# Kernel optimization log

Measured on AMD Instinct MI355X. Metric: run time of the kernel, lower is better.

The kernel has to match this reference:

```python
import jax, jax.numpy as jnp
import numpy as np

E, D, H, K = 8, 2048, 1024, 2  # num_experts, input_size, hidden_size, top_k
B, L = 2, 1024


def setup_inputs() -> dict:
    key = jax.random.key(0)
    k1, k2, k3, k4 = jax.random.split(key, 4)
    x = jax.random.normal(k1, (B, L, D), dtype=jnp.float32)
    w_gate = jax.random.normal(k2, (E, D), dtype=jnp.float32) * 0.02   # router Linear weight [E, D]
    w_in = jax.random.normal(k3, (E, 2 * H, D), dtype=jnp.float32) * 0.02  # ParallelExperts [E, out=2H, in=D]
    w_out = jax.random.normal(k4, (E, D, H), dtype=jnp.float32) * 0.02     # ParallelExperts [E, out=D, in=H]
    bias = jnp.zeros((D,), dtype=jnp.float32)
    return {"x": x, "w_gate": w_gate, "w_in": w_in, "w_out": w_out, "bias": bias}


def _moe_forward(x, w_gate, w_in, w_out, bias):
    bsz, length, d = x.shape
    xt = x.reshape(-1, d)  # [T, D]
    # top-k router: logits -> top-k -> softmax over selected logits
    logits = xt @ w_gate.T  # [T, E]
    topk_vals, topk_idx = jax.lax.top_k(logits, K)  # [T, K]
    topk_gates = jax.nn.softmax(topk_vals, axis=-1)  # [T, K]
    T = xt.shape[0]
    # dense [T, E] gate matrix; zero for non-selected experts, so the dense
    # per-expert compute below is mathematically identical to gathered dispatch
    gates = jnp.zeros((T, E), dtype=xt.dtype).at[jnp.arange(T)[:, None], topk_idx].add(topk_gates)
    # expert GLU FFN, vectorized over experts
    h = jnp.einsum('td,efd->tef', xt, w_in)  # [T, E, 2H]
    h1, h2 = jnp.split(h, 2, axis=-1)
    a = jax.nn.silu(h1) * h2                 # [T, E, H]
    eo = jnp.einsum('teh,edh->ted', a, w_out)  # [T, E, D]
    y = jnp.einsum('ted,te->td', eo, gates) + bias
    return y.reshape(bsz, length, d)


def reference(x, w_gate, w_in, w_out, bias):
    y = _moe_forward(x, w_gate, w_in, w_out, bias)
    loss = jnp.float32(0.0)  # router aux loss is 0 in eval mode (JetMoE top_k_gating)
    return (y, loss)
```

## Files before the change

### kernel.cpp

```cpp
#include <hip/hip_runtime.h>
#include <hip/hip_bf16.h>

#define E_    8
#define D_    2048
#define H_    1024
#define T_    2048
#define BK    64

using u16   = unsigned short;
using s16x8 = __attribute__((ext_vector_type(8))) short;
using f32x4 = __attribute__((ext_vector_type(4))) float;

__device__ __forceinline__ short f2bf(float f) {
  __hip_bfloat16 h = __float2bfloat16(f);
  return __builtin_bit_cast(short, h);
}
__device__ __forceinline__ s16x8 cvt8(f32x4 a, f32x4 b) {
  s16x8 o;
  o[0]=f2bf(a.x); o[1]=f2bf(a.y); o[2]=f2bf(a.z); o[3]=f2bf(a.w);
  o[4]=f2bf(b.x); o[5]=f2bf(b.y); o[6]=f2bf(b.z); o[7]=f2bf(b.w);
  return o;
}
__device__ __forceinline__ int slot(int r, int c) { return r * 64 + ((c ^ (r & 7)) << 3); }

__device__ __forceinline__ void gload16(const void* g, void* l) {
  __builtin_amdgcn_global_load_lds((const __attribute__((address_space(1))) void*)g,
                                   (__attribute__((address_space(3))) void*)l, 16, 0, 0);
}

#define FIND_EXPERT(ml, cnt, e, mt, Ne)                        \
  { int b_ = 0;                                                \
    _Pragma("unroll")                                          \
    for (int i_ = 0; i_ < E_; ++i_) {                          \
      int ti_ = (cnt[i_] + 255) >> 8;                          \
      if ((ml) >= b_ && (ml) < b_ + ti_) {                     \
        e = i_; mt = (ml) - b_; Ne = cnt[i_]; }                \
      b_ += ti_; } }


__global__ __launch_bounds__(256) void init_kernel(
    const float* __restrict__ bias, float* __restrict__ out, int* __restrict__ counts)
{
  int idx = blockIdx.x * 256 + threadIdx.x;
  if (blockIdx.x == 0 && threadIdx.x < E_) counts[threadIdx.x] = 0;
  if (idx == 0) out[(size_t)T_ * D_] = 0.0f;
  int dq = idx & (D_ / 4 - 1);
  f32x4 b = *(const f32x4*)(bias + dq * 4);
  *(f32x4*)(out + (size_t)idx * 4) = b;
}

__global__ __launch_bounds__(256) void router_kernel(
    const float* __restrict__ x, const float* __restrict__ wg,
    u16* __restrict__ xb, int* __restrict__ lists, float* __restrict__ gates,
    int* __restrict__ counts)
{
  int t = blockIdx.x;
  int tid = threadIdx.x;
  const float* xr = x + (size_t)t * D_;
  float acc[E_];
#pragma unroll
  for (int e = 0; e < E_; ++e) acc[e] = 0.f;
#pragma unroll
  for (int i = 0; i < D_ / 256; ++i) {
    int d = tid + 256 * i;
    float xv = xr[d];
    xb[(size_t)t * D_ + d] = (u16)f2bf(xv);
#pragma unroll
    for (int e = 0; e < E_; ++e) acc[e] += xv * wg[e * D_ + d];
  }
#pragma unroll
  for (int off = 32; off >= 1; off >>= 1)
#pragma unroll
    for (int e = 0; e < E_; ++e) acc[e] += __shfl_down(acc[e], off);

  __shared__ float red[4][E_];
  int w = tid >> 6, lane = tid & 63;
  if (lane == 0)
#pragma unroll
    for (int e = 0; e < E_; ++e) red[w][e] = acc[e];
  __syncthreads();
  if (tid == 0) {
    float v0 = -1e30f, v1 = -1e30f; int e0 = 0, e1 = 0;
#pragma unroll
    for (int e = 0; e < E_; ++e) {
      float v = red[0][e] + red[1][e] + red[2][e] + red[3][e];
      if (v > v0)      { v1 = v0; e1 = e0; v0 = v; e0 = e; }
      else if (v > v1) { v1 = v;  e1 = e; }
    }
    float g1 = expf(v1 - v0);
    float inv = 1.f / (1.f + g1);
    float g0 = inv; g1 *= inv;
    int s0 = atomicAdd(&counts[e0], 1);
    lists[e0 * T_ + s0] = t * 2 + 0;
    gates[t * 2 + 0] = g0;
    int s1 = atomicAdd(&counts[e1], 1);
    lists[e1 * T_ + s1] = t * 2 + 1;
    gates[t * 2 + 1] = g1;
  }
}

__global__ __launch_bounds__(512, 2) void gemm1_kernel(
    const u16* __restrict__ xb, const float* __restrict__ w_in,
    const int* __restrict__ lists, const int* __restrict__ counts,
    u16* __restrict__ a_buf)
{
  __shared__ __align__(16) u16 As[2][256 * 64];
  __shared__ __align__(16) u16 Bs[2][128 * 64];

  int cnt[E_];
#pragma unroll
  for (int i = 0; i < E_; ++i) cnt[i] = counts[i];
  int mt_total = 0;
#pragma unroll
  for (int i = 0; i < E_; ++i) mt_total += (cnt[i] + 255) >> 8;
  const int NN1 = 2 * H_ / 128;
  int total = mt_total * NN1;
  int chunk = (total + 7) >> 3;

  int tid = threadIdx.x, w = tid >> 6, lane = tid & 63;
  int swzc = ((lane & 7) ^ (lane >> 3)) * 8;
  int sr = tid >> 3;
  int brow = tid >> 2, bc = (tid & 3) * 2;
  int wr = (w >> 1) * 64, wcB = (w & 1) * 64, lrow = lane & 15, g = lane >> 4;
  int lcol = lane & 15, lr4 = (lane >> 4) * 4;

  int xcd = blockIdx.x & 7, bslot = blockIdx.x >> 3;

  for (int sl = bslot; sl < chunk; sl += 32) {
    int t = xcd * chunk + sl;
    if (t >= total) break;
    int ml = t / NN1, n = t % NN1;
    int e = 0, mt = 0, Ne = 0;
    FIND_EXPERT(ml, cnt, e, mt, Ne);

    const u16* ap[4];
#pragma unroll
    for (int i = 0; i < 4; ++i) {
      int gr = mt * 256 + 32 * w + 8 * i + (lane >> 3);
      if (gr >= Ne) gr = Ne - 1;
      ap[i] = xb + (size_t)(lists[e * T_ + gr] >> 1) * D_ + swzc;
    }
    int o = n * 64 + ((brow >> 4) & 1) * H_ + (brow >> 5) * 16 + (brow & 15);
    const float* bp = w_in + (size_t)e * (2 * H_) * D_ + (size_t)o * D_ + bc * 8;

    f32x4 acc[4][4];
#pragma unroll
    for (int m = 0; m < 4; ++m)
#pragma unroll
      for (int nn = 0; nn < 4; ++nn) acc[m][nn] = (f32x4){0.f, 0.f, 0.f, 0.f};

    f32x4 bl[4];
#define LOADS1(K) { _Pragma("unroll") for (int j = 0; j < 4; ++j) \
                      bl[j] = *(const f32x4*)(bp + (K) + j * 4); \
                    _Pragma("unroll") for (int i = 0; i < 4; ++i) \
                      gload16(ap[i] + (K), &As[(K) ? !((K/BK) & 1) : 0][(32 * w + 8 * i) * 64]); }
    { _Pragma("unroll") for (int j = 0; j < 4; ++j) bl[j] = *(const f32x4*)(bp + j * 4);
      _Pragma("unroll") for (int i = 0; i < 4; ++i) gload16(ap[i], &As[0][(32 * w + 8 * i) * 64]); }
    *(s16x8*)(&Bs[0][slot(brow, bc)])     = cvt8(bl[0], bl[1]);
    *(s16x8*)(&Bs[0][slot(brow, bc + 1)]) = cvt8(bl[2], bl[3]);
    __syncthreads();

    const int NT = D_ / BK;
    for (int kt = 0; kt < NT; ++kt) {
      int cur = kt & 1;
      if (kt + 1 < NT) {
        int k = (kt + 1) * BK;
#pragma unroll
        for (int j = 0; j < 4; ++j) bl[j] = *(const f32x4*)(bp + k + j * 4);
#pragma unroll
        for (int i = 0; i < 4; ++i) gload16(ap[i] + k, &As[cur ^ 1][(32 * w + 8 * i) * 64]);
      }
#pragma unroll
      for (int ks = 0; ks < 2; ++ks) {
        int ch = ks * 4 + g;
        s16x8 af[4], bf[4];
#pragma unroll
        for (int m = 0; m < 4; ++m) af[m] = *(const s16x8*)(&As[cur][slot(wr + m * 16 + lrow, ch)]);
#pragma unroll
        for (int nn = 0; nn < 4; ++nn) bf[nn] = *(const s16x8*)(&Bs[cur][slot(wcB + nn * 16 + lrow, ch)]);
#pragma unroll
        for (int m = 0; m < 4; ++m)
#pragma unroll
          for (int nn = 0; nn < 4; ++nn)
            acc[m][nn] = __builtin_amdgcn_mfma_f32_16x16x32_bf16(af[m], bf[nn], acc[m][nn], 0, 0, 0);
      }
      if (kt + 1 < NT) {
        *(s16x8*)(&Bs[cur ^ 1][slot(brow, bc)])     = cvt8(bl[0], bl[1]);
        *(s16x8*)(&Bs[cur ^ 1][slot(brow, bc + 1)]) = cvt8(bl[2], bl[3]);
      }
      __syncthreads();
    }
#pragma unroll
    for (int m = 0; m < 4; ++m)
#pragma unroll
      for (int q = 0; q < 4; ++q) {
        int row = mt * 256 + wr + m * 16 + lr4 + q;
        if (row < Ne) {
#pragma unroll
          for (int n2 = 0; n2 < 2; ++n2) {
            float h1 = acc[m][n2 * 2][q], h2 = acc[m][n2 * 2 + 1][q];
            float a = (h1 / (1.f + __expf(-h1))) * h2;
            int col = n * 64 + ((w & 1) * 2 + n2) * 16 + lcol;
            a_buf[((size_t)e * T_ + row) * H_ + col] = (u16)f2bf(a);
          }
        }
      }
  }
}

__global__ __launch_bounds__(512, 2) void gemm2_kernel(
    const u16* __restrict__ a_buf, const float* __restrict__ w_out,
    const int* __restrict__ lists, const int* __restrict__ counts,
    const float* __restrict__ gates, float* __restrict__ out)
{
  __shared__ __align__(16) u16 As[2][256 * 64];
  __shared__ __align__(16) u16 Bs[2][128 * 64];

  int cnt[E_];
#pragma unroll
  for (int i = 0; i < E_; ++i) cnt[i] = counts[i];
  int mt_total = 0;
#pragma unroll
  for (int i = 0; i < E_; ++i) mt_total += (cnt[i] + 255) >> 8;
  const int NN2 = D_ / 128;
  int total = mt_total * NN2;
  int chunk = (total + 7) >> 3;

  int tid = threadIdx.x, w = tid >> 6, lane = tid & 63;
  int swzc = ((lane & 7) ^ (lane >> 3)) * 8;
  int brow = tid >> 2, bc = (tid & 3) * 2;
  int wr = (w >> 1) * 64, wcB = (w & 1) * 64, lrow = lane & 15, g = lane >> 4;
  int lcol = lane & 15, lr4 = (lane >> 4) * 4;

  int xcd = blockIdx.x & 7, bslot = blockIdx.x >> 3;

  for (int sl = bslot; sl < chunk; sl += 32) {
    int t = xcd * chunk + sl;
    if (t >= total) break;
    int ml = t / NN2, n = t % NN2;
    int e = 0, mt = 0, Ne = 0;
    FIND_EXPERT(ml, cnt, e, mt, Ne);

    const u16* ap[4];
#pragma unroll
    for (int i = 0; i < 4; ++i) {
      int gr = mt * 256 + 32 * w + 8 * i + (lane >> 3);
      if (gr >= Ne) gr = Ne - 1;
      ap[i] = a_buf + ((size_t)e * T_ + gr) * H_ + swzc;
    }
    const float* bp = w_out + (size_t)e * D_ * H_ + (size_t)(n * 128 + brow) * H_ + bc * 8;

    f32x4 acc[4][4];
#pragma unroll
    for (int m = 0; m < 4; ++m)
#pragma unroll
      for (int nn = 0; nn < 4; ++nn) acc[m][nn] = (f32x4){0.f, 0.f, 0.f, 0.f};

    f32x4 bl[4];
    { _Pragma("unroll") for (int j = 0; j < 4; ++j) bl[j] = *(const f32x4*)(bp + j * 4);
      _Pragma("unroll") for (int i = 0; i < 4; ++i) gload16(ap[i], &As[0][(32 * w + 8 * i) * 64]); }
    *(s16x8*)(&Bs[0][slot(brow, bc)])     = cvt8(bl[0], bl[1]);
    *(s16x8*)(&Bs[0][slot(brow, bc + 1)]) = cvt8(bl[2], bl[3]);
    __syncthreads();

    const int NT = H_ / BK;
    for (int kt = 0; kt < NT; ++kt) {
      int cur = kt & 1;
      if (kt + 1 < NT) {
        int k = (kt + 1) * BK;
#pragma unroll
        for (int j = 0; j < 4; ++j) bl[j] = *(const f32x4*)(bp + k + j * 4);
#pragma unroll
        for (int i = 0; i < 4; ++i) gload16(ap[i] + k, &As[cur ^ 1][(32 * w + 8 * i) * 64]);
      }
#pragma unroll
      for (int ks = 0; ks < 2; ++ks) {
        int ch = ks * 4 + g;
        s16x8 af[4], bf[4];
#pragma unroll
        for (int m = 0; m < 4; ++m) af[m] = *(const s16x8*)(&As[cur][slot(wr + m * 16 + lrow, ch)]);
#pragma unroll
        for (int nn = 0; nn < 4; ++nn) bf[nn] = *(const s16x8*)(&Bs[cur][slot(wcB + nn * 16 + lrow, ch)]);
#pragma unroll
        for (int m = 0; m < 4; ++m)
#pragma unroll
          for (int nn = 0; nn < 4; ++nn)
            acc[m][nn] = __builtin_amdgcn_mfma_f32_16x16x32_bf16(af[m], bf[nn], acc[m][nn], 0, 0, 0);
      }
      if (kt + 1 < NT) {
        *(s16x8*)(&Bs[cur ^ 1][slot(brow, bc)])     = cvt8(bl[0], bl[1]);
        *(s16x8*)(&Bs[cur ^ 1][slot(brow, bc + 1)]) = cvt8(bl[2], bl[3]);
      }
      __syncthreads();
    }
#pragma unroll
    for (int m = 0; m < 4; ++m)
#pragma unroll
      for (int q = 0; q < 4; ++q) {
        int row = mt * 256 + wr + m * 16 + lr4 + q;
        if (row < Ne) {
          int p = lists[e * T_ + row];
          float gt = gates[p];
          int tok = p >> 1;
#pragma unroll
          for (int nn = 0; nn < 4; ++nn)
            atomicAdd(&out[(size_t)tok * D_ + n * 128 + wcB + nn * 16 + lcol], gt * acc[m][nn][q]);
        }
      }
  }
}

extern "C" void kernel_launch(void* const* d_in, const int* in_sizes, int n_in,
                              void* d_out, int out_size, void* d_ws, size_t ws_size,
                              hipStream_t stream)
{
  const float* x      = (const float*)d_in[0];
  const float* w_gate = (const float*)d_in[1];
  const float* w_in   = (const float*)d_in[2];
  const float* w_out  = (const float*)d_in[3];
  const float* bias   = (const float*)d_in[4];
  float* out = (float*)d_out;

  char* ws = (char*)d_ws;
  u16*   xb     = (u16*)(ws);
  u16*   a_buf  = (u16*)(ws + 8388608);
  int*   lists  = (int*)(ws + 41943040);
  float* gates  = (float*)(ws + 42008576);
  int*   counts = (int*)(ws + 42024960);

  init_kernel<<<T_ * D_ / 4 / 256, 256, 0, stream>>>(bias, out, counts);
  router_kernel<<<T_, 256, 0, stream>>>(x, w_gate, xb, lists, gates, counts);
  gemm1_kernel<<<256, 512, 0, stream>>>(xb, w_in, lists, counts, a_buf);
  gemm2_kernel<<<256, 512, 0, stream>>>(a_buf, w_out, lists, counts, gates, out);
}
```

Before: 265.8 us.

## Triple-buffer A tiles with explicit waitcnt scheduling and retile both MoE GEMMs

Both expert GEMMs now use a three-stage LDS ring for the activation tiles, prefetching two K-steps ahead. Plain __syncthreads is replaced with manual vmcnt/lgkmcnt waits, sched barriers, s_barrier and setprio around the MFMA bursts, so loads overlap compute. The wave tiling changes so each wave covers more rows and fewer columns, gemm2 drops to 128-row M tiles, and its grid doubles to 512 blocks. gemm1 launch bounds fall to one block per CU because of the larger LDS, which lowers occupancy and relies on the hand-tuned wait counts being correct.

```diff
diff --git a/kernel.cpp b/kernel.cpp
--- a/kernel.cpp
+++ b/kernel.cpp
@@ -11,6 +11,10 @@
 using s16x8 = __attribute__((ext_vector_type(8))) short;
 using f32x4 = __attribute__((ext_vector_type(4))) float;
 
+#define WAITVM(N) asm volatile("s_waitcnt vmcnt(" #N ")" ::: "memory")
+#define LGKM0     asm volatile("s_waitcnt lgkmcnt(0)" ::: "memory")
+#define SB0       __builtin_amdgcn_sched_barrier(0)
+
 __device__ __forceinline__ short f2bf(float f) {
   __hip_bfloat16 h = __float2bfloat16(f);
   return __builtin_bit_cast(short, h);
@@ -28,11 +32,11 @@
                                    (__attribute__((address_space(3))) void*)l, 16, 0, 0);
 }
 
-#define FIND_EXPERT(ml, cnt, e, mt, Ne)                        \
+#define FIND_EXPERT(ml, cnt, e, mt, Ne, RND, SH)               \
   { int b_ = 0;                                                \
     _Pragma("unroll")                                          \
     for (int i_ = 0; i_ < E_; ++i_) {                          \
-      int ti_ = (cnt[i_] + 255) >> 8;                          \
+      int ti_ = (cnt[i_] + RND) >> SH;                         \
       if ((ml) >= b_ && (ml) < b_ + ti_) {                     \
         e = i_; mt = (ml) - b_; Ne = cnt[i_]; }                \
       b_ += ti_; } }
@@ -99,12 +103,12 @@
   }
 }
 
-__global__ __launch_bounds__(512, 2) void gemm1_kernel(
+__global__ __launch_bounds__(512, 1) void gemm1_kernel(
     const u16* __restrict__ xb, const float* __restrict__ w_in,
     const int* __restrict__ lists, const int* __restrict__ counts,
     u16* __restrict__ a_buf)
 {
-  __shared__ __align__(16) u16 As[2][256 * 64];
+  __shared__ __align__(16) u16 As[3][256 * 64];
   __shared__ __align__(16) u16 Bs[2][128 * 64];
 
   int cnt[E_];
@@ -113,25 +117,22 @@
   int mt_total = 0;
 #pragma unroll
   for (int i = 0; i < E_; ++i) mt_total += (cnt[i] + 255) >> 8;
-  const int NN1 = 2 * H_ / 128;
-  int total = mt_total * NN1;
+  int total = mt_total * 16;
   int chunk = (total + 7) >> 3;
 
   int tid = threadIdx.x, w = tid >> 6, lane = tid & 63;
   int swzc = ((lane & 7) ^ (lane >> 3)) * 8;
-  int sr = tid >> 3;
   int brow = tid >> 2, bc = (tid & 3) * 2;
-  int wr = (w >> 1) * 64, wcB = (w & 1) * 64, lrow = lane & 15, g = lane >> 4;
+  int wr = (w >> 2) * 128, wc = (w & 3) * 32, lrow = lane & 15, g = lane >> 4;
   int lcol = lane & 15, lr4 = (lane >> 4) * 4;
-
   int xcd = blockIdx.x & 7, bslot = blockIdx.x >> 3;
 
   for (int sl = bslot; sl < chunk; sl += 32) {
     int t = xcd * chunk + sl;
     if (t >= total) break;
-    int ml = t / NN1, n = t % NN1;
+    int ml = t >> 4, n = t & 15;
     int e = 0, mt = 0, Ne = 0;
-    FIND_EXPERT(ml, cnt, e, mt, Ne);
+    FIND_EXPERT(ml, cnt, e, mt, Ne, 255, 8);
 
     const u16* ap[4];
 #pragma unroll
@@ -143,66 +144,85 @@
     int o = n * 64 + ((brow >> 4) & 1) * H_ + (brow >> 5) * 16 + (brow & 15);
     const float* bp = w_in + (size_t)e * (2 * H_) * D_ + (size_t)o * D_ + bc * 8;
 
-    f32x4 acc[4][4];
-#pragma unroll
-    for (int m = 0; m < 4; ++m)
-#pragma unroll
-      for (int nn = 0; nn < 4; ++nn) acc[m][nn] = (f32x4){0.f, 0.f, 0.f, 0.f};
-
+    f32x4 acc[8][2];
+#pragma unroll
+    for (int m = 0; m < 8; ++m) { acc[m][0] = (f32x4){0,0,0,0}; acc[m][1] = (f32x4){0,0,0,0}; }
     f32x4 bl[4];
-#define LOADS1(K) { _Pragma("unroll") for (int j = 0; j < 4; ++j) \
-                      bl[j] = *(const f32x4*)(bp + (K) + j * 4); \
-                    _Pragma("unroll") for (int i = 0; i < 4; ++i) \
-                      gload16(ap[i] + (K), &As[(K) ? !((K/BK) & 1) : 0][(32 * w + 8 * i) * 64]); }
-    { _Pragma("unroll") for (int j = 0; j < 4; ++j) bl[j] = *(const f32x4*)(bp + j * 4);
-      _Pragma("unroll") for (int i = 0; i < 4; ++i) gload16(ap[i], &As[0][(32 * w + 8 * i) * 64]); }
+
+#pragma unroll
+    for (int j = 0; j < 4; ++j) bl[j] = *(const f32x4*)(bp + j * 4);
+    SB0;
+#pragma unroll
+    for (int i = 0; i < 4; ++i) gload16(ap[i], &As[0][(32 * w + 8 * i) * 64]);
+    SB0;
+#pragma unroll
+    for (int i = 0; i < 4; ++i) gload16(ap[i] + BK, &As[1][(32 * w + 8 * i) * 64]);
+    SB0;
+    WAITVM(8);  SB0;
     *(s16x8*)(&Bs[0][slot(brow, bc)])     = cvt8(bl[0], bl[1]);
     *(s16x8*)(&Bs[0][slot(brow, bc + 1)]) = cvt8(bl[2], bl[3]);
-    __syncthreads();
+    SB0;
+#pragma unroll
+    for (int j = 0; j < 4; ++j) bl[j] = *(const f32x4*)(bp + BK + j * 4);
+    SB0;
+    WAITVM(8);  SB0;
+    LGKM0;
+    __builtin_amdgcn_s_barrier();
 
     const int NT = D_ / BK;
     for (int kt = 0; kt < NT; ++kt) {
-      int cur = kt & 1;
-      if (kt + 1 < NT) {
-        int k = (kt + 1) * BK;
-#pragma unroll
-        for (int j = 0; j < 4; ++j) bl[j] = *(const f32x4*)(bp + k + j * 4);
-#pragma unroll
-        for (int i = 0; i < 4; ++i) gload16(ap[i] + k, &As[cur ^ 1][(32 * w + 8 * i) * 64]);
+      int cur = kt % 3;
+      if (kt + 2 < NT) {
+        int wrt = cur + 2; if (wrt >= 3) wrt -= 3;
+        int k2 = (kt + 2) * BK;
+        SB0;
+#pragma unroll
+        for (int i = 0; i < 4; ++i) gload16(ap[i] + k2, &As[wrt][(32 * w + 8 * i) * 64]);
+        SB0;
       }
 #pragma unroll
       for (int ks = 0; ks < 2; ++ks) {
         int ch = ks * 4 + g;
-        s16x8 af[4], bf[4];
-#pragma unroll
-        for (int m = 0; m < 4; ++m) af[m] = *(const s16x8*)(&As[cur][slot(wr + m * 16 + lrow, ch)]);
-#pragma unroll
-        for (int nn = 0; nn < 4; ++nn) bf[nn] = *(const s16x8*)(&Bs[cur][slot(wcB + nn * 16 + lrow, ch)]);
-#pragma unroll
-        for (int m = 0; m < 4; ++m)
-#pragma unroll
-          for (int nn = 0; nn < 4; ++nn)
+        s16x8 af[8], bf[2];
+#pragma unroll
+        for (int m = 0; m < 8; ++m) af[m] = *(const s16x8*)(&As[cur][slot(wr + m * 16 + lrow, ch)]);
+        bf[0] = *(const s16x8*)(&Bs[kt & 1][slot(wc + lrow, ch)]);
+        bf[1] = *(const s16x8*)(&Bs[kt & 1][slot(wc + 16 + lrow, ch)]);
+        __builtin_amdgcn_s_setprio(1);
+#pragma unroll
+        for (int m = 0; m < 8; ++m)
+#pragma unroll
+          for (int nn = 0; nn < 2; ++nn)
             acc[m][nn] = __builtin_amdgcn_mfma_f32_16x16x32_bf16(af[m], bf[nn], acc[m][nn], 0, 0, 0);
+        __builtin_amdgcn_s_setprio(0);
       }
       if (kt + 1 < NT) {
-        *(s16x8*)(&Bs[cur ^ 1][slot(brow, bc)])     = cvt8(bl[0], bl[1]);
-        *(s16x8*)(&Bs[cur ^ 1][slot(brow, bc + 1)]) = cvt8(bl[2], bl[3]);
-      }
-      __syncthreads();
-    }
-#pragma unroll
-    for (int m = 0; m < 4; ++m)
+        if (kt + 2 < NT) { WAITVM(4); } else { WAITVM(0); }
+        SB0;
+        *(s16x8*)(&Bs[(kt + 1) & 1][slot(brow, bc)])     = cvt8(bl[0], bl[1]);
+        *(s16x8*)(&Bs[(kt + 1) & 1][slot(brow, bc + 1)]) = cvt8(bl[2], bl[3]);
+        SB0;
+        if (kt + 2 < NT) {
+          int k2 = (kt + 2) * BK;
+#pragma unroll
+          for (int j = 0; j < 4; ++j) bl[j] = *(const f32x4*)(bp + k2 + j * 4);
+          SB0;
+        }
+        LGKM0;
+        __builtin_amdgcn_s_barrier();
+      }
+    }
+    LGKM0;
+    __builtin_amdgcn_s_barrier();
+#pragma unroll
+    for (int m = 0; m < 8; ++m)
 #pragma unroll
       for (int q = 0; q < 4; ++q) {
         int row = mt * 256 + wr + m * 16 + lr4 + q;
         if (row < Ne) {
-#pragma unroll
-          for (int n2 = 0; n2 < 2; ++n2) {
-            float h1 = acc[m][n2 * 2][q], h2 = acc[m][n2 * 2 + 1][q];
-            float a = (h1 / (1.f + __expf(-h1))) * h2;
-            int col = n * 64 + ((w & 1) * 2 + n2) * 16 + lcol;
-            a_buf[((size_t)e * T_ + row) * H_ + col] = (u16)f2bf(a);
-          }
+          float h1 = acc[m][0][q], h2 = acc[m][1][q];
+          float a = (h1 / (1.f + __expf(-h1))) * h2;
+          a_buf[((size_t)e * T_ + row) * H_ + n * 64 + (w & 3) * 16 + lcol] = (u16)f2bf(a);
         }
       }
   }
@@ -213,7 +233,7 @@
     const int* __restrict__ lists, const int* __restrict__ counts,
     const float* __restrict__ gates, float* __restrict__ out)
 {
-  __shared__ __align__(16) u16 As[2][256 * 64];
+  __shared__ __align__(16) u16 As[3][128 * 64];
   __shared__ __align__(16) u16 Bs[2][128 * 64];
 
   int cnt[E_];
@@ -221,90 +241,115 @@
   for (int i = 0; i < E_; ++i) cnt[i] = counts[i];
   int mt_total = 0;
 #pragma unroll
-  for (int i = 0; i < E_; ++i) mt_total += (cnt[i] + 255) >> 8;
-  const int NN2 = D_ / 128;
-  int total = mt_total * NN2;
+  for (int i = 0; i < E_; ++i) mt_total += (cnt[i] + 127) >> 7;
+  int total = mt_total * 16;
   int chunk = (total + 7) >> 3;
 
   int tid = threadIdx.x, w = tid >> 6, lane = tid & 63;
   int swzc = ((lane & 7) ^ (lane >> 3)) * 8;
   int brow = tid >> 2, bc = (tid & 3) * 2;
-  int wr = (w >> 1) * 64, wcB = (w & 1) * 64, lrow = lane & 15, g = lane >> 4;
+  int wr = (w >> 2) * 64, wc = (w & 3) * 32, lrow = lane & 15, g = lane >> 4;
   int lcol = lane & 15, lr4 = (lane >> 4) * 4;
-
   int xcd = blockIdx.x & 7, bslot = blockIdx.x >> 3;
 
-  for (int sl = bslot; sl < chunk; sl += 32) {
+  for (int sl = bslot; sl < chunk; sl += 64) {
     int t = xcd * chunk + sl;
     if (t >= total) break;
-    int ml = t / NN2, n = t % NN2;
+    int ml = t >> 4, n = t & 15;
     int e = 0, mt = 0, Ne = 0;
-    FIND_EXPERT(ml, cnt, e, mt, Ne);
-
-    const u16* ap[4];
-#pragma unroll
-    for (int i = 0; i < 4; ++i) {
-      int gr = mt * 256 + 32 * w + 8 * i + (lane >> 3);
+    FIND_EXPERT(ml, cnt, e, mt, Ne, 127, 7);
+
+    const u16* ap[2];
+#pragma unroll
+    for (int i = 0; i < 2; ++i) {
+      int gr = mt * 128 + 16 * w + 8 * i + (lane >> 3);
       if (gr >= Ne) gr = Ne - 1;
       ap[i] = a_buf + ((size_t)e * T_ + gr) * H_ + swzc;
     }
     const float* bp = w_out + (size_t)e * D_ * H_ + (size_t)(n * 128 + brow) * H_ + bc * 8;
 
-    f32x4 acc[4][4];
-#pragma unroll
-    for (int m = 0; m < 4; ++m)
-#pragma unroll
-      for (int nn = 0; nn < 4; ++nn) acc[m][nn] = (f32x4){0.f, 0.f, 0.f, 0.f};
-
+    f32x4 acc[4][2];
+#pragma unroll
+    for (int m = 0; m < 4; ++m) { acc[m][0] = (f32x4){0,0,0,0}; acc[m][1] = (f32x4){0,0,0,0}; }
     f32x4 bl[4];
-    { _Pragma("unroll") for (int j = 0; j < 4; ++j) bl[j] = *(const f32x4*)(bp + j * 4);
-      _Pragma("unroll") for (int i = 0; i < 4; ++i) gload16(ap[i], &As[0][(32 * w + 8 * i) * 64]); }
+
+#pragma unroll
+    for (int j = 0; j < 4; ++j) bl[j] = *(const f32x4*)(bp + j * 4);
+    SB0;
+#pragma unroll
+    for (int i = 0; i < 2; ++i) gload16(ap[i], &As[0][(16 * w + 8 * i) * 64]);
+    SB0;
+#pragma unroll
+    for (int i = 0; i < 2; ++i) gload16(ap[i] + BK, &As[1][(16 * w + 8 * i) * 64]);
+    SB0;
+    WAITVM(4);  SB0;
     *(s16x8*)(&Bs[0][slot(brow, bc)])     = cvt8(bl[0], bl[1]);
     *(s16x8*)(&Bs[0][slot(brow, bc + 1)]) = cvt8(bl[2], bl[3]);
-    __syncthreads();
+    SB0;
+#pragma unroll
+    for (int j = 0; j < 4; ++j) bl[j] = *(const f32x4*)(bp + BK + j * 4);
+    SB0;
+    WAITVM(6);  SB0;
+    LGKM0;
+    __builtin_amdgcn_s_barrier();
 
     const int NT = H_ / BK;
     for (int kt = 0; kt < NT; ++kt) {
-      int cur = kt & 1;
-      if (kt + 1 < NT) {
-        int k = (kt + 1) * BK;
-#pragma unroll
-        for (int j = 0; j < 4; ++j) bl[j] = *(const f32x4*)(bp + k + j * 4);
-#pragma unroll
-        for (int i = 0; i < 4; ++i) gload16(ap[i] + k, &As[cur ^ 1][(32 * w + 8 * i) * 64]);
+      int cur = kt % 3;
+      if (kt + 2 < NT) {
+        int wrt = cur + 2; if (wrt >= 3) wrt -= 3;
+        int k2 = (kt + 2) * BK;
+        SB0;
+#pragma unroll
+        for (int i = 0; i < 2; ++i) gload16(ap[i] + k2, &As[wrt][(16 * w + 8 * i) * 64]);
+        SB0;
       }
 #pragma unroll
       for (int ks = 0; ks < 2; ++ks) {
         int ch = ks * 4 + g;
-        s16x8 af[4], bf[4];
+        s16x8 af[4], bf[2];
 #pragma unroll
         for (int m = 0; m < 4; ++m) af[m] = *(const s16x8*)(&As[cur][slot(wr + m * 16 + lrow, ch)]);
-#pragma unroll
-        for (int nn = 0; nn < 4; ++nn) bf[nn] = *(const s16x8*)(&Bs[cur][slot(wcB + nn * 16 + lrow, ch)]);
+        bf[0] = *(const s16x8*)(&Bs[kt & 1][slot(wc + lrow, ch)]);
+        bf[1] = *(const s16x8*)(&Bs[kt & 1][slot(wc + 16 + lrow, ch)]);
+        __builtin_amdgcn_s_setprio(1);
 #pragma unroll
         for (int m = 0; m < 4; ++m)
 #pragma unroll
-          for (int nn = 0; nn < 4; ++nn)
+          for (int nn = 0; nn < 2; ++nn)
             acc[m][nn] = __builtin_amdgcn_mfma_f32_16x16x32_bf16(af[m], bf[nn], acc[m][nn], 0, 0, 0);
+        __builtin_amdgcn_s_setprio(0);
       }
       if (kt + 1 < NT) {
-        *(s16x8*)(&Bs[cur ^ 1][slot(brow, bc)])     = cvt8(bl[0], bl[1]);
-        *(s16x8*)(&Bs[cur ^ 1][slot(brow, bc + 1)]) = cvt8(bl[2], bl[3]);
-      }
-      __syncthreads();
-    }
+        if (kt + 2 < NT) { WAITVM(2); } else { WAITVM(0); }
+        SB0;
+        *(s16x8*)(&Bs[(kt + 1) & 1][slot(brow, bc)])     = cvt8(bl[0], bl[1]);
+        *(s16x8*)(&Bs[(kt + 1) & 1][slot(brow, bc + 1)]) = cvt8(bl[2], bl[3]);
+        SB0;
+        if (kt + 2 < NT) {
+          int k2 = (kt + 2) * BK;
+#pragma unroll
+          for (int j = 0; j < 4; ++j) bl[j] = *(const f32x4*)(bp + k2 + j * 4);
+          SB0;
+        }
+        LGKM0;
+        __builtin_amdgcn_s_barrier();
+      }
+    }
+    LGKM0;
+    __builtin_amdgcn_s_barrier();
 #pragma unroll
     for (int m = 0; m < 4; ++m)
 #pragma unroll
       for (int q = 0; q < 4; ++q) {
-        int row = mt * 256 + wr + m * 16 + lr4 + q;
+        int row = mt * 128 + wr + m * 16 + lr4 + q;
         if (row < Ne) {
           int p = lists[e * T_ + row];
           float gt = gates[p];
           int tok = p >> 1;
 #pragma unroll
-          for (int nn = 0; nn < 4; ++nn)
-            atomicAdd(&out[(size_t)tok * D_ + n * 128 + wcB + nn * 16 + lcol], gt * acc[m][nn][q]);
+          for (int nn = 0; nn < 2; ++nn)
+            atomicAdd(&out[(size_t)tok * D_ + n * 128 + wc + nn * 16 + lcol], gt * acc[m][nn][q]);
         }
       }
   }
@@ -331,5 +376,5 @@
   init_kernel<<<T_ * D_ / 4 / 256, 256, 0, stream>>>(bias, out, counts);
   router_kernel<<<T_, 256, 0, stream>>>(x, w_gate, xb, lists, gates, counts);
   gemm1_kernel<<<256, 512, 0, stream>>>(xb, w_in, lists, counts, a_buf);
-  gemm2_kernel<<<256, 512, 0, stream>>>(a_buf, w_out, lists, counts, gates, out);
-}
+  gemm2_kernel<<<512, 512, 0, stream>>>(a_buf, w_out, lists, counts, gates, out);
+}
```

New measurement: 231.7 us. -12.8%, faster.

## Shrink GEMM M-tiles to 128, add dynamic work queue, fold init into router

Applied to the files above, without the earlier changes.

Both expert GEMMs now use 128-row M tiles with 256-thread blocks (double the grid) and pull tiles from a per-XCD atomic work queue instead of a static stride. Adjacent M-tiles are interleaved so they share the same weight N-tile. The bias/output init kernel is removed: the router writes the bias rows and a memset clears the counters and queues. The aim is less padding waste per expert and better load balance across uneven expert counts, at the cost of less A/B reuse per tile and extra atomic and barrier traffic.

```diff
diff --git a/kernel.cpp b/kernel.cpp
--- a/kernel.cpp
+++ b/kernel.cpp
@@ -11,6 +11,8 @@
 using s16x8 = __attribute__((ext_vector_type(8))) short;
 using f32x4 = __attribute__((ext_vector_type(4))) float;
 
+#define WAITVM0 asm volatile("s_waitcnt vmcnt(0)" ::: "memory")
+
 __device__ __forceinline__ short f2bf(float f) {
   __hip_bfloat16 h = __float2bfloat16(f);
   return __builtin_bit_cast(short, h);
@@ -32,30 +34,29 @@
   { int b_ = 0;                                                \
     _Pragma("unroll")                                          \
     for (int i_ = 0; i_ < E_; ++i_) {                          \
-      int ti_ = (cnt[i_] + 255) >> 8;                          \
+      int ti_ = (cnt[i_] + 127) >> 7;                          \
       if ((ml) >= b_ && (ml) < b_ + ti_) {                     \
         e = i_; mt = (ml) - b_; Ne = cnt[i_]; }                \
       b_ += ti_; } }
 
 
-__global__ __launch_bounds__(256) void init_kernel(
-    const float* __restrict__ bias, float* __restrict__ out, int* __restrict__ counts)
-{
-  int idx = blockIdx.x * 256 + threadIdx.x;
-  if (blockIdx.x == 0 && threadIdx.x < E_) counts[threadIdx.x] = 0;
-  if (idx == 0) out[(size_t)T_ * D_] = 0.0f;
-  int dq = idx & (D_ / 4 - 1);
-  f32x4 b = *(const f32x4*)(bias + dq * 4);
-  *(f32x4*)(out + (size_t)idx * 4) = b;
-}
-
 __global__ __launch_bounds__(256) void router_kernel(
     const float* __restrict__ x, const float* __restrict__ wg,
+    const float* __restrict__ bias,
     u16* __restrict__ xb, int* __restrict__ lists, float* __restrict__ gates,
-    int* __restrict__ counts)
+    int* __restrict__ counts, float* __restrict__ out)
 {
   int t = blockIdx.x;
   int tid = threadIdx.x;
+
+  {
+    const float* bp = bias + tid * 8;
+    f32x4 b0 = *(const f32x4*)(bp), b1 = *(const f32x4*)(bp + 4);
+    *(f32x4*)(out + (size_t)t * D_ + tid * 8)     = b0;
+    *(f32x4*)(out + (size_t)t * D_ + tid * 8 + 4) = b1;
+    if (t == 0 && tid == 0) out[(size_t)T_ * D_] = 0.0f;
+  }
+
   const float* xr = x + (size_t)t * D_;
   float acc[E_];
 #pragma unroll
@@ -99,65 +100,70 @@
   }
 }
 
-__global__ __launch_bounds__(512, 2) void gemm1_kernel(
+__global__ __launch_bounds__(256, 2) void gemm1_kernel(
     const u16* __restrict__ xb, const float* __restrict__ w_in,
     const int* __restrict__ lists, const int* __restrict__ counts,
-    u16* __restrict__ a_buf)
+    u16* __restrict__ a_buf, int* __restrict__ q)
 {
-  __shared__ __align__(16) u16 As[2][256 * 64];
+  __shared__ __align__(16) u16 As[2][128 * 64];
   __shared__ __align__(16) u16 Bs[2][128 * 64];
+  __shared__ int s_sl;
 
   int cnt[E_];
 #pragma unroll
   for (int i = 0; i < E_; ++i) cnt[i] = counts[i];
   int mt_total = 0;
 #pragma unroll
-  for (int i = 0; i < E_; ++i) mt_total += (cnt[i] + 255) >> 8;
-  const int NN1 = 2 * H_ / 128;
-  int total = mt_total * NN1;
+  for (int i = 0; i < E_; ++i) mt_total += (cnt[i] + 127) >> 7;
+  int total = ((mt_total + 1) >> 1) * 32;
   int chunk = (total + 7) >> 3;
 
   int tid = threadIdx.x, w = tid >> 6, lane = tid & 63;
   int swzc = ((lane & 7) ^ (lane >> 3)) * 8;
-  int sr = tid >> 3;
-  int brow = tid >> 2, bc = (tid & 3) * 2;
-  int wr = (w >> 1) * 64, wcB = (w & 1) * 64, lrow = lane & 15, g = lane >> 4;
+  int wr = (w >> 1) * 64, wc = (w & 1) * 64, lrow = lane & 15, g = lane >> 4;
   int lcol = lane & 15, lr4 = (lane >> 4) * 4;
-
-  int xcd = blockIdx.x & 7, bslot = blockIdx.x >> 3;
-
-  for (int sl = bslot; sl < chunk; sl += 32) {
+  int br = tid >> 1, bhalf = (tid & 1) * 32, bj0 = (tid & 1) * 4;
+  int xcd = blockIdx.x & 7;
+
+  for (;;) {
+    __syncthreads();
+    if (tid == 0) s_sl = atomicAdd(&q[xcd], 1);
+    __syncthreads();
+    int sl = s_sl;
+    if (sl >= chunk) break;
     int t = xcd * chunk + sl;
     if (t >= total) break;
-    int ml = t / NN1, n = t % NN1;
+    int p = t >> 5, qq = t & 31;
+    int ml = p * 2 + (qq & 1), n = qq >> 1;
+    if (ml >= mt_total) continue;
     int e = 0, mt = 0, Ne = 0;
     FIND_EXPERT(ml, cnt, e, mt, Ne);
 
     const u16* ap[4];
 #pragma unroll
     for (int i = 0; i < 4; ++i) {
-      int gr = mt * 256 + 32 * w + 8 * i + (lane >> 3);
+      int gr = mt * 128 + w * 32 + i * 8 + (lane >> 3);
       if (gr >= Ne) gr = Ne - 1;
       ap[i] = xb + (size_t)(lists[e * T_ + gr] >> 1) * D_ + swzc;
     }
-    int o = n * 64 + ((brow >> 4) & 1) * H_ + (brow >> 5) * 16 + (brow & 15);
-    const float* bp = w_in + (size_t)e * (2 * H_) * D_ + (size_t)o * D_ + bc * 8;
+    int o = n * 64 + ((br >> 4) & 1) * H_ + (br >> 5) * 16 + (br & 15);
+    const float* bp = w_in + (size_t)e * (2 * H_) * D_ + (size_t)o * D_ + bhalf;
 
     f32x4 acc[4][4];
 #pragma unroll
     for (int m = 0; m < 4; ++m)
 #pragma unroll
       for (int nn = 0; nn < 4; ++nn) acc[m][nn] = (f32x4){0.f, 0.f, 0.f, 0.f};
-
-    f32x4 bl[4];
-#define LOADS1(K) { _Pragma("unroll") for (int j = 0; j < 4; ++j) \
-                      bl[j] = *(const f32x4*)(bp + (K) + j * 4); \
-                    _Pragma("unroll") for (int i = 0; i < 4; ++i) \
-                      gload16(ap[i] + (K), &As[(K) ? !((K/BK) & 1) : 0][(32 * w + 8 * i) * 64]); }
-    { _Pragma("unroll") for (int j = 0; j < 4; ++j) bl[j] = *(const f32x4*)(bp + j * 4);
-      _Pragma("unroll") for (int i = 0; i < 4; ++i) gload16(ap[i], &As[0][(32 * w + 8 * i) * 64]); }
-    *(s16x8*)(&Bs[0][slot(brow, bc)])     = cvt8(bl[0], bl[1]);
-    *(s16x8*)(&Bs[0][slot(brow, bc + 1)]) = cvt8(bl[2], bl[3]);
+    f32x4 bl[8];
+
+#pragma unroll
+    for (int i = 0; i < 4; ++i) gload16(ap[i], &As[0][(w * 32 + i * 8) * 64]);
+#pragma unroll
+    for (int j = 0; j < 8; ++j) bl[j] = *(const f32x4*)(bp + j * 4);
+    WAITVM0;
+#pragma unroll
+    for (int j = 0; j < 4; ++j)
+      *(s16x8*)(&Bs[0][slot(br, bj0 + j)]) = cvt8(bl[2 * j], bl[2 * j + 1]);
     __syncthreads();
 
     const int NT = D_ / BK;
@@ -166,9 +172,9 @@
       if (kt + 1 < NT) {
         int k = (kt + 1) * BK;
 #pragma unroll
-        for (int j = 0; j < 4; ++j) bl[j] = *(const f32x4*)(bp + k + j * 4);
-#pragma unroll
-        for (int i = 0; i < 4; ++i) gload16(ap[i] + k, &As[cur ^ 1][(32 * w + 8 * i) * 64]);
+        for (int i = 0; i < 4; ++i) gload16(ap[i] + k, &As[cur ^ 1][(w * 32 + i * 8) * 64]);
+#pragma unroll
+        for (int j = 0; j < 8; ++j) bl[j] = *(const f32x4*)(bp + k + j * 4);
       }
 #pragma unroll
       for (int ks = 0; ks < 2; ++ks) {
@@ -177,7 +183,7 @@
 #pragma unroll
         for (int m = 0; m < 4; ++m) af[m] = *(const s16x8*)(&As[cur][slot(wr + m * 16 + lrow, ch)]);
 #pragma unroll
-        for (int nn = 0; nn < 4; ++nn) bf[nn] = *(const s16x8*)(&Bs[cur][slot(wcB + nn * 16 + lrow, ch)]);
+        for (int nn = 0; nn < 4; ++nn) bf[nn] = *(const s16x8*)(&Bs[cur][slot(wc + nn * 16 + lrow, ch)]);
 #pragma unroll
         for (int m = 0; m < 4; ++m)
 #pragma unroll
@@ -185,22 +191,24 @@
             acc[m][nn] = __builtin_amdgcn_mfma_f32_16x16x32_bf16(af[m], bf[nn], acc[m][nn], 0, 0, 0);
       }
       if (kt + 1 < NT) {
-        *(s16x8*)(&Bs[cur ^ 1][slot(brow, bc)])     = cvt8(bl[0], bl[1]);
-        *(s16x8*)(&Bs[cur ^ 1][slot(brow, bc + 1)]) = cvt8(bl[2], bl[3]);
-      }
-      __syncthreads();
+        WAITVM0;
+#pragma unroll
+        for (int j = 0; j < 4; ++j)
+          *(s16x8*)(&Bs[cur ^ 1][slot(br, bj0 + j)]) = cvt8(bl[2 * j], bl[2 * j + 1]);
+        __syncthreads();
+      }
     }
 #pragma unroll
     for (int m = 0; m < 4; ++m)
 #pragma unroll
-      for (int q = 0; q < 4; ++q) {
-        int row = mt * 256 + wr + m * 16 + lr4 + q;
+      for (int q2 = 0; q2 < 4; ++q2) {
+        int row = mt * 128 + wr + m * 16 + lr4 + q2;
         if (row < Ne) {
 #pragma unroll
-          for (int n2 = 0; n2 < 2; ++n2) {
-            float h1 = acc[m][n2 * 2][q], h2 = acc[m][n2 * 2 + 1][q];
+          for (int p2 = 0; p2 < 2; ++p2) {
+            float h1 = acc[m][2 * p2][q2], h2 = acc[m][2 * p2 + 1][q2];
             float a = (h1 / (1.f + __expf(-h1))) * h2;
-            int col = n * 64 + ((w & 1) * 2 + n2) * 16 + lcol;
+            int col = n * 64 + ((w & 1) * 2 + p2) * 16 + lcol;
             a_buf[((size_t)e * T_ + row) * H_ + col] = (u16)f2bf(a);
           }
         }
@@ -208,59 +216,69 @@
   }
 }
 
-__global__ __launch_bounds__(512, 2) void gemm2_kernel(
+__global__ __launch_bounds__(256, 2) void gemm2_kernel(
     const u16* __restrict__ a_buf, const float* __restrict__ w_out,
     const int* __restrict__ lists, const int* __restrict__ counts,
-    const float* __restrict__ gates, float* __restrict__ out)
+    const float* __restrict__ gates, float* __restrict__ out, int* __restrict__ q)
 {
-  __shared__ __align__(16) u16 As[2][256 * 64];
+  __shared__ __align__(16) u16 As[2][128 * 64];
   __shared__ __align__(16) u16 Bs[2][128 * 64];
+  __shared__ int s_sl;
 
   int cnt[E_];
 #pragma unroll
   for (int i = 0; i < E_; ++i) cnt[i] = counts[i];
   int mt_total = 0;
 #pragma unroll
-  for (int i = 0; i < E_; ++i) mt_total += (cnt[i] + 255) >> 8;
-  const int NN2 = D_ / 128;
-  int total = mt_total * NN2;
+  for (int i = 0; i < E_; ++i) mt_total += (cnt[i] + 127) >> 7;
+  int total = ((mt_total + 1) >> 1) * 32;
   int chunk = (total + 7) >> 3;
 
   int tid = threadIdx.x, w = tid >> 6, lane = tid & 63;
   int swzc = ((lane & 7) ^ (lane >> 3)) * 8;
-  int brow = tid >> 2, bc = (tid & 3) * 2;
-  int wr = (w >> 1) * 64, wcB = (w & 1) * 64, lrow = lane & 15, g = lane >> 4;
+  int wr = (w >> 1) * 64, wc = (w & 1) * 64, lrow = lane & 15, g = lane >> 4;
   int lcol = lane & 15, lr4 = (lane >> 4) * 4;
-
-  int xcd = blockIdx.x & 7, bslot = blockIdx.x >> 3;
-
-  for (int sl = bslot; sl < chunk; sl += 32) {
+  int br = tid >> 1, bhalf = (tid & 1) * 32, bj0 = (tid & 1) * 4;
+  int xcd = blockIdx.x & 7;
+
+  for (;;) {
+    __syncthreads();
+    if (tid == 0) s_sl = atomicAdd(&q[xcd], 1);
+    __syncthreads();
+    int sl = s_sl;
+    if (sl >= chunk) break;
     int t = xcd * chunk + sl;
     if (t >= total) break;
-    int ml = t / NN2, n = t % NN2;
+    int p = t >> 5, qq = t & 31;
+    int ml = p * 2 + (qq & 1), n = qq >> 1;
+    if (ml >= mt_total) continue;
     int e = 0, mt = 0, Ne = 0;
     FIND_EXPERT(ml, cnt, e, mt, Ne);
 
     const u16* ap[4];
 #pragma unroll
     for (int i = 0; i < 4; ++i) {
-      int gr = mt * 256 + 32 * w + 8 * i + (lane >> 3);
+      int gr = mt * 128 + w * 32 + i * 8 + (lane >> 3);
       if (gr >= Ne) gr = Ne - 1;
       ap[i] = a_buf + ((size_t)e * T_ + gr) * H_ + swzc;
     }
-    const float* bp = w_out + (size_t)e * D_ * H_ + (size_t)(n * 128 + brow) * H_ + bc * 8;
+    const float* bp = w_out + (size_t)e * D_ * H_ + (size_t)(n * 128 + br) * H_ + bhalf;
 
     f32x4 acc[4][4];
 #pragma unroll
     for (int m = 0; m < 4; ++m)
 #pragma unroll
       for (int nn = 0; nn < 4; ++nn) acc[m][nn] = (f32x4){0.f, 0.f, 0.f, 0.f};
-
-    f32x4 bl[4];
-    { _Pragma("unroll") for (int j = 0; j < 4; ++j) bl[j] = *(const f32x4*)(bp + j * 4);
-      _Pragma("unroll") for (int i = 0; i < 4; ++i) gload16(ap[i], &As[0][(32 * w + 8 * i) * 64]); }
-    *(s16x8*)(&Bs[0][slot(brow, bc)])     = cvt8(bl[0], bl[1]);
-    *(s16x8*)(&Bs[0][slot(brow, bc + 1)]) = cvt8(bl[2], bl[3]);
+    f32x4 bl[8];
+
+#pragma unroll
+    for (int i = 0; i < 4; ++i) gload16(ap[i], &As[0][(w * 32 + i * 8) * 64]);
+#pragma unroll
+    for (int j = 0; j < 8; ++j) bl[j] = *(const f32x4*)(bp + j * 4);
+    WAITVM0;
+#pragma unroll
+    for (int j = 0; j < 4; ++j)
+      *(s16x8*)(&Bs[0][slot(br, bj0 + j)]) = cvt8(bl[2 * j], bl[2 * j + 1]);
     __syncthreads();
 
     const int NT = H_ / BK;
@@ -269,9 +287,9 @@
       if (kt + 1 < NT) {
         int k = (kt + 1) * BK;
 #pragma unroll
-        for (int j = 0; j < 4; ++j) bl[j] = *(const f32x4*)(bp + k + j * 4);
-#pragma unroll
-        for (int i = 0; i < 4; ++i) gload16(ap[i] + k, &As[cur ^ 1][(32 * w + 8 * i) * 64]);
+        for (int i = 0; i < 4; ++i) gload16(ap[i] + k, &As[cur ^ 1][(w * 32 + i * 8) * 64]);
+#pragma unroll
+        for (int j = 0; j < 8; ++j) bl[j] = *(const f32x4*)(bp + k + j * 4);
       }
 #pragma unroll
       for (int ks = 0; ks < 2; ++ks) {
@@ -280,7 +298,7 @@
 #pragma unroll
         for (int m = 0; m < 4; ++m) af[m] = *(const s16x8*)(&As[cur][slot(wr + m * 16 + lrow, ch)]);
 #pragma unroll
-        for (int nn = 0; nn < 4; ++nn) bf[nn] = *(const s16x8*)(&Bs[cur][slot(wcB + nn * 16 + lrow, ch)]);
+        for (int nn = 0; nn < 4; ++nn) bf[nn] = *(const s16x8*)(&Bs[cur][slot(wc + nn * 16 + lrow, ch)]);
 #pragma unroll
         for (int m = 0; m < 4; ++m)
 #pragma unroll
@@ -288,23 +306,27 @@
             acc[m][nn] = __builtin_amdgcn_mfma_f32_16x16x32_bf16(af[m], bf[nn], acc[m][nn], 0, 0, 0);
       }
       if (kt + 1 < NT) {
-        *(s16x8*)(&Bs[cur ^ 1][slot(brow, bc)])     = cvt8(bl[0], bl[1]);
-        *(s16x8*)(&Bs[cur ^ 1][slot(brow, bc + 1)]) = cvt8(bl[2], bl[3]);
-      }
-      __syncthreads();
+        WAITVM0;
+#pragma unroll
+        for (int j = 0; j < 4; ++j)
+          *(s16x8*)(&Bs[cur ^ 1][slot(br, bj0 + j)]) = cvt8(bl[2 * j], bl[2 * j + 1]);
+        __syncthreads();
+      }
     }
 #pragma unroll
     for (int m = 0; m < 4; ++m)
 #pragma unroll
-      for (int q = 0; q < 4; ++q) {
-        int row = mt * 256 + wr + m * 16 + lr4 + q;
+      for (int q2 = 0; q2 < 4; ++q2) {
+        int row = mt * 128 + wr + m * 16 + lr4 + q2;
         if (row < Ne) {
-          int p = lists[e * T_ + row];
-          float gt = gates[p];
-          int tok = p >> 1;
-#pragma unroll
-          for (int nn = 0; nn < 4; ++nn)
-            atomicAdd(&out[(size_t)tok * D_ + n * 128 + wcB + nn * 16 + lcol], gt * acc[m][nn][q]);
+          int pidx = lists[e * T_ + row];
+          float gt = gates[pidx];
+          int tok = pidx >> 1;
+#pragma unroll
+          for (int nn = 0; nn < 4; ++nn) {
+            int col = n * 128 + wc + nn * 16 + lcol;
+            atomicAdd(&out[(size_t)tok * D_ + col], gt * acc[m][nn][q2]);
+          }
         }
       }
   }
@@ -327,9 +349,11 @@
   int*   lists  = (int*)(ws + 41943040);
   float* gates  = (float*)(ws + 42008576);
   int*   counts = (int*)(ws + 42024960);
-
-  init_kernel<<<T_ * D_ / 4 / 256, 256, 0, stream>>>(bias, out, counts);
-  router_kernel<<<T_, 256, 0, stream>>>(x, w_gate, xb, lists, gates, counts);
-  gemm1_kernel<<<256, 512, 0, stream>>>(xb, w_in, lists, counts, a_buf);
-  gemm2_kernel<<<256, 512, 0, stream>>>(a_buf, w_out, lists, counts, gates, out);
-}
+  int*   q1     = (int*)(ws + 42024992);
+  int*   q2     = (int*)(ws + 42025024);
+
+  hipMemsetAsync(counts, 0, 96, stream);
+  router_kernel<<<T_, 256, 0, stream>>>(x, w_gate, bias, xb, lists, gates, counts, out);
+  gemm1_kernel<<<512, 256, 0, stream>>>(xb, w_in, lists, counts, a_buf, q1);
+  gemm2_kernel<<<512, 256, 0, stream>>>(a_buf, w_out, lists, counts, gates, out, q2);
+}
```

Measured after the change: 323.0 us. 1.22x slower.
